# Optimization experiments

Hardware: AMD Instinct MI355X
Metric: run time of the kernel (lower is better)

The kernel has to match this reference:

```python
import jax, jax.numpy as jnp
import numpy as np

NU, NI, D, B, L, E = 100000, 50000, 128, 3, 2, 1500000
N = NU + NI  # total nodes
EPS = 1e-5


def setup_inputs() -> dict:
    key = jax.random.key(0)
    ks = jax.random.split(key, 20)
    s = 0.05  # xavier-ish scale for 128-dim layers
    inp = {}
    inp["edge_index"] = jax.random.randint(ks[0], (2, E), 0, N, dtype=jnp.int32)
    inp["edge_type"] = jax.random.randint(ks[1], (E,), 0, B, dtype=jnp.int32)
    inp["item_feats"] = jax.random.normal(ks[2], (NI, D), jnp.float32)
    inp["user_emb"] = jax.random.normal(ks[3], (NU, D), jnp.float32) * s
    inp["user_proj_W"] = jax.random.normal(ks[4], (D, D), jnp.float32) * s
    inp["user_proj_b"] = jnp.zeros((D,), jnp.float32)
    inp["item_proj_W"] = jax.random.normal(ks[5], (D, D), jnp.float32) * s
    inp["item_proj_b"] = jnp.zeros((D,), jnp.float32)
    # stacked SAGEConv params: lin_l (neighbor, with bias) and lin_r (root, no bias)
    inp["sage_Wl"] = jax.random.normal(ks[6], (B, L, D, D), jnp.float32) * s
    inp["sage_bl"] = jnp.zeros((B, L, D), jnp.float32)
    inp["sage_Wr"] = jax.random.normal(ks[7], (B, L, D, D), jnp.float32) * s
    inp["bn_gamma"] = jnp.ones((B, L, D), jnp.float32)
    inp["bn_beta"] = jnp.zeros((B, L, D), jnp.float32)
    inp["query_W"] = jax.random.normal(ks[8], (D, D), jnp.float32) * s
    inp["query_b"] = jnp.zeros((D,), jnp.float32)
    inp["key_W"] = jax.random.normal(ks[9], (B, D, D), jnp.float32) * s
    inp["key_b"] = jnp.zeros((B, D), jnp.float32)
    inp["fuse_W"] = jax.random.normal(ks[10], (D, D), jnp.float32) * s
    inp["fuse_b"] = jnp.zeros((D,), jnp.float32)
    inp["refine_W"] = jax.random.normal(ks[11], (D, D), jnp.float32) * s
    inp["refine_b"] = jnp.zeros((D,), jnp.float32)
    return inp


def reference(edge_index, edge_type, item_feats, user_emb,
              user_proj_W, user_proj_b, item_proj_W, item_proj_b,
              sage_Wl, sage_bl, sage_Wr, bn_gamma, bn_beta,
              query_W, query_b, key_W, key_b,
              fuse_W, fuse_b, refine_W, refine_b):
    # initial node features: projected user embeddings + projected item feats
    x = jnp.concatenate([user_emb @ user_proj_W + user_proj_b,
                         item_feats @ item_proj_W + item_proj_b], axis=0)  # [N, D]
    src, dst = edge_index[0], edge_index[1]
    outs = []
    for b in range(B):
        # redirect edges of other behaviours to a dummy segment N (dropped)
        dst_b = jnp.where(edge_type == b, dst, N)
        cnt = jax.ops.segment_sum(jnp.ones((E,), x.dtype), dst_b, num_segments=N + 1)[:N]
        denom = jnp.maximum(cnt, 1.0)[:, None]
        h = x
        for l in range(L):
            # SAGEConv: mean-aggregate neighbor messages + root transform
            agg = jax.ops.segment_sum(h[src], dst_b, num_segments=N + 1)[:N] / denom
            h = agg @ sage_Wl[b, l] + sage_bl[b, l] + h @ sage_Wr[b, l]
            # BatchNorm1d (training-mode batch statistics, biased variance)
            mu = h.mean(axis=0)
            var = h.var(axis=0)
            h = (h - mu) * jax.lax.rsqrt(var + EPS) * bn_gamma[b, l] + bn_beta[b, l]
            if l < L - 1:
                h = jax.nn.relu(h)
        outs.append(x + h)  # residual
    stack = jnp.stack(outs, axis=0)  # [B, N, D]
    # attention fusion across behaviours
    Q = x @ query_W + query_b                                   # [N, D]
    K = jnp.einsum('bnd,bde->bne', stack, key_W) + key_b[:, None, :]  # [B, N, D]
    logits = jnp.einsum('nd,bnd->nb', Q, K)                      # [N, B]
    w = jax.nn.softmax(logits, axis=-1)
    fused = jnp.einsum('nb,bnd->nd', w, stack)
    fused = fused @ fuse_W + fuse_b
    # refine: Linear + ReLU (dropout is identity in eval)
    return jax.nn.relu(fused @ refine_W + refine_b)
```

## Files before the change

kernel.cpp:

```cpp
#include <hip/hip_runtime.h>

#define NUSER 100000
#define NITEM 50000
#define NNODE 150000
#define DIM 128
#define NB 3
#define NL 2
#define BN_EPS 1e-5f
#define NT3P 450560
#define SCAN_BLOCKS 440
#define TILESN 2344
#define BNBLK 18750
#define BNABLK 9375

typedef unsigned short u16;
typedef _Float16 f16;
typedef __attribute__((ext_vector_type(8))) _Float16 f16x8;
typedef __attribute__((ext_vector_type(8))) unsigned short us8;
typedef __attribute__((ext_vector_type(4))) float f32x4;

__device__ __forceinline__ float h2f(u16 u) { f16 h; __builtin_memcpy(&h, &u, 2); return (float)h; }
__device__ __forceinline__ u16 f2h(float f) { f16 h = (f16)f; u16 u; __builtin_memcpy(&u, &h, 2); return u; }

struct Out3 { u16* p[3]; };
struct WPtrs { const float* s[8]; };


__global__ __launch_bounds__(256) void count_edges(const int* __restrict__ ei,
                                                   const int* __restrict__ et, int E,
                                                   int* __restrict__ cnt) {
    int t = blockIdx.x * 256 + threadIdx.x;
    if (t >= E) return;
    atomicAdd(&cnt[et[t] * NNODE + ei[E + t]], 1);
}

__global__ __launch_bounds__(256) void scan1(const int* __restrict__ cnt, int* __restrict__ bsum) {
    __shared__ int sh[256];
    int tid = threadIdx.x;
    int base = blockIdx.x * 1024 + tid * 4;
    int4 v = *(const int4*)(cnt + base);
    sh[tid] = v.x + v.y + v.z + v.w;
    __syncthreads();
    for (int off = 128; off > 0; off >>= 1) {
        if (tid < off) sh[tid] += sh[tid + off];
        __syncthreads();
    }
    if (tid == 0) bsum[blockIdx.x] = sh[0];
}

__global__ __launch_bounds__(512) void scan2(int* __restrict__ bsum, int nb) {
    __shared__ int sh[512];
    int tid = threadIdx.x;
    sh[tid] = (tid < nb) ? bsum[tid] : 0;
    __syncthreads();
    for (int off = 1; off < 512; off <<= 1) {
        int v = sh[tid];
        int add = (tid >= off) ? sh[tid - off] : 0;
        __syncthreads();
        sh[tid] = v + add;
        __syncthreads();
    }
    if (tid < nb) bsum[tid] = (tid == 0) ? 0 : sh[tid - 1];
}

__global__ __launch_bounds__(256) void scan3(const int* __restrict__ cnt, const int* __restrict__ bsum,
                                             int* __restrict__ row_start, int* __restrict__ cur) {
    __shared__ int sh[256];
    int tid = threadIdx.x;
    int base = blockIdx.x * 1024 + tid * 4;
    int4 v = *(const int4*)(cnt + base);
    sh[tid] = v.x + v.y + v.z + v.w;
    __syncthreads();
    for (int off = 1; off < 256; off <<= 1) {
        int a = sh[tid];
        int add = (tid >= off) ? sh[tid - off] : 0;
        __syncthreads();
        sh[tid] = a + add;
        __syncthreads();
    }
    int excl = ((tid == 0) ? 0 : sh[tid - 1]) + bsum[blockIdx.x];
    int4 o;
    o.x = excl; o.y = excl + v.x; o.z = o.y + v.y; o.w = o.z + v.z;
    *(int4*)(row_start + base) = o;
    *(int4*)(cur + base) = o;
}

__global__ __launch_bounds__(256) void scatter_csr(const int* __restrict__ ei,
                                                   const int* __restrict__ et, int E,
                                                   int* __restrict__ cur, int* __restrict__ adj) {
    int t = blockIdx.x * 256 + threadIdx.x;
    if (t >= E) return;
    int pos = atomicAdd(&cur[et[t] * NNODE + ei[E + t]], 1);
    adj[pos] = ei[t];
}


__global__ __launch_bounds__(256) void wconv_all(WPtrs w, u16* __restrict__ dst) {
    int gid = blockIdx.x * 256 + threadIdx.x;
    if (gid >= 20 * 16384) return;
    int m = gid >> 14, idx = gid & 16383;
    int k = idx & 127, n = idx >> 7;
    const float* src; int li;
    if (m == 0)       { src = w.s[0]; li = 0; }
    else if (m == 1)  { src = w.s[1]; li = 0; }
    else if (m < 8)   { src = w.s[2]; li = m - 2; }
    else if (m < 14)  { src = w.s[3]; li = m - 8; }
    else if (m == 14) { src = w.s[4]; li = 0; }
    else if (m < 18)  { src = w.s[5]; li = m - 15; }
    else if (m == 18) { src = w.s[6]; li = 0; }
    else              { src = w.s[7]; li = 0; }
    dst[(size_t)m * 16384 + idx] = f2h(src[(size_t)li * 16384 + k * 128 + n]);
}


__global__ __launch_bounds__(256) void bn_apply(u16* __restrict__ h,
                                                const float* __restrict__ stats6,
                                                const float* __restrict__ gamma,
                                                const float* __restrict__ beta) {
    __shared__ float sc[DIM];
    __shared__ float sf[DIM];
    const int tid = threadIdx.x;
    const int b = blockIdx.x / BNABLK;
    const int blk = blockIdx.x % BNABLK;
    const int bl = b * NL;
    if (tid < DIM) {
        const float* st = stats6 + bl * 256;
        const float invN = 1.0f / (float)NNODE;
        float mu = st[tid] * invN;
        float var = fmaxf(st[DIM + tid] * invN - mu * mu, 0.f);
        float scv = gamma[bl * DIM + tid] * rsqrtf(var + BN_EPS);
        sc[tid] = scv;
        sf[tid] = beta[bl * DIM + tid] - mu * scv;
    }
    __syncthreads();
    const int i = blk * 256 + tid;
    const int c8 = (i & 15) * 8;
    u16* p = h + (size_t)b * NNODE * DIM + (size_t)i * 8;
    us8 u = *(const us8*)p;
    us8 o;
#pragma unroll
    for (int j = 0; j < 8; ++j)
        o[j] = f2h(fmaxf(h2f(u[j]) * sc[c8 + j] + sf[c8 + j], 0.f));
    *(us8*)p = o;
}


__global__ __launch_bounds__(256, 5) void sage_layer(
    const u16* __restrict__ hin0, const u16* __restrict__ wt_Wl,
    const u16* __restrict__ wt_Wr, const float* __restrict__ sage_bl,
    float* __restrict__ stats6, Out3 outs, int layer,
    const int* __restrict__ adj, const int* __restrict__ row_start,
    const int* __restrict__ cnt) {
    __shared__ u16 T1[64][136];
    __shared__ float sstat[256];
    const int tid = threadIdx.x;
    const int b = blockIdx.x / TILESN;
    const int tile = blockIdx.x % TILESN;
    const int r0 = tile * 64;
    const int bl = b * NL + layer;
    const u16* hin = hin0 + (layer ? (size_t)b * NNODE * DIM : 0);
    const u16* Wl = wt_Wl + (size_t)bl * 16384;
    const u16* Wr = wt_Wr + (size_t)bl * 16384;

    sstat[tid] = 0.f;

    {
        const int row = tid >> 2;
        const int c0 = (tid & 3) * 32;
        float a[32];
#pragma unroll
        for (int j = 0; j < 32; ++j) a[j] = 0.f;
        const int n = r0 + row;
        if (n < NNODE) {
            const int base = b * NNODE + n;
            const int s0 = row_start[base];
            const int deg = cnt[base];
            int e = 0;
            for (; e + 1 < deg; e += 2) {
                const u16* p1 = hin + (size_t)adj[s0 + e] * DIM + c0;
                const u16* p2 = hin + (size_t)adj[s0 + e + 1] * DIM + c0;
                us8 u0 = *(const us8*)p1;
                us8 u1 = *(const us8*)(p1 + 8);
                us8 u2 = *(const us8*)(p1 + 16);
                us8 u3 = *(const us8*)(p1 + 24);
                us8 v0 = *(const us8*)p2;
                us8 v1 = *(const us8*)(p2 + 8);
                us8 v2 = *(const us8*)(p2 + 16);
                us8 v3 = *(const us8*)(p2 + 24);
#pragma unroll
                for (int j = 0; j < 8; ++j) {
                    a[j]      += h2f(u0[j]) + h2f(v0[j]);
                    a[8 + j]  += h2f(u1[j]) + h2f(v1[j]);
                    a[16 + j] += h2f(u2[j]) + h2f(v2[j]);
                    a[24 + j] += h2f(u3[j]) + h2f(v3[j]);
                }
            }
            if (e < deg) {
                const u16* p1 = hin + (size_t)adj[s0 + e] * DIM + c0;
                us8 u0 = *(const us8*)p1;
                us8 u1 = *(const us8*)(p1 + 8);
                us8 u2 = *(const us8*)(p1 + 16);
                us8 u3 = *(const us8*)(p1 + 24);
#pragma unroll
                for (int j = 0; j < 8; ++j) {
                    a[j]      += h2f(u0[j]);
                    a[8 + j]  += h2f(u1[j]);
                    a[16 + j] += h2f(u2[j]);
                    a[24 + j] += h2f(u3[j]);
                }
            }
            const float s = 1.0f / (float)(deg > 1 ? deg : 1);
#pragma unroll
            for (int j = 0; j < 32; ++j) a[j] *= s;
        }
#pragma unroll
        for (int k = 0; k < 4; ++k) {
            us8 o;
#pragma unroll
            for (int j = 0; j < 8; ++j) o[j] = f2h(a[8 * k + j]);
            *(us8*)&T1[row][c0 + 8 * k] = o;
        }
    }
    __syncthreads();

    const int wave = tid >> 6, lane = tid & 63, q = lane >> 4, rlo = lane & 15;
    const f16x8 zf = (f16x8)(f16)0.f;
    f32x4 acc[4][2];
#pragma unroll
    for (int t = 0; t < 4; ++t) { acc[t][0] = (f32x4)0.f; acc[t][1] = (f32x4)0.f; }
#pragma unroll
    for (int kc = 0; kc < DIM; kc += 32) {
        f16x8 b1v[2], b2v[2];
#pragma unroll
        for (int c = 0; c < 2; ++c) {
            b1v[c] = *(const f16x8*)(Wl + (size_t)(wave * 32 + 16 * c + rlo) * DIM + kc + q * 8);
            b2v[c] = *(const f16x8*)(Wr + (size_t)(wave * 32 + 16 * c + rlo) * DIM + kc + q * 8);
        }
#pragma unroll
        for (int t = 0; t < 4; ++t) {
            f16x8 a1 = *(const f16x8*)&T1[16 * t + rlo][kc + q * 8];
            int rr = r0 + 16 * t + rlo;
            f16x8 a2 = (rr < NNODE) ? *(const f16x8*)(hin + (size_t)rr * DIM + kc + q * 8) : zf;
            acc[t][0] = __builtin_amdgcn_mfma_f32_16x16x32_f16(a1, b1v[0], acc[t][0], 0, 0, 0);
            acc[t][1] = __builtin_amdgcn_mfma_f32_16x16x32_f16(a1, b1v[1], acc[t][1], 0, 0, 0);
            acc[t][0] = __builtin_amdgcn_mfma_f32_16x16x32_f16(a2, b2v[0], acc[t][0], 0, 0, 0);
            acc[t][1] = __builtin_amdgcn_mfma_f32_16x16x32_f16(a2, b2v[1], acc[t][1], 0, 0, 0);
        }
    }

    const int col0 = wave * 32 + rlo, col1 = col0 + 16;
    const float bb0 = sage_bl[bl * DIM + col0], bb1 = sage_bl[bl * DIM + col1];
    u16* C = outs.p[b];
    float rs0 = 0, rq0 = 0, rs1 = 0, rq1 = 0;
#pragma unroll
    for (int t = 0; t < 4; ++t) {
#pragma unroll
        for (int r = 0; r < 4; ++r) {
            int row = r0 + 16 * t + q * 4 + r;
            if (row >= NNODE) continue;
            float v0 = acc[t][0][r] + bb0;
            float v1 = acc[t][1][r] + bb1;
            rs0 += v0; rq0 += v0 * v0; rs1 += v1; rq1 += v1 * v1;
            C[(size_t)row * DIM + col0] = f2h(v0);
            C[(size_t)row * DIM + col1] = f2h(v1);
        }
    }
    rs0 += __shfl_xor(rs0, 16); rs0 += __shfl_xor(rs0, 32);
    rq0 += __shfl_xor(rq0, 16); rq0 += __shfl_xor(rq0, 32);
    rs1 += __shfl_xor(rs1, 16); rs1 += __shfl_xor(rs1, 32);
    rq1 += __shfl_xor(rq1, 16); rq1 += __shfl_xor(rq1, 32);
    if (q == 0) {
        atomicAdd(&sstat[col0], rs0);
        atomicAdd(&sstat[DIM + col0], rq0);
        atomicAdd(&sstat[col1], rs1);
        atomicAdd(&sstat[DIM + col1], rq1);
    }
    __syncthreads();
    if (tid < DIM) {
        float* so = stats6 + bl * 256;
        atomicAdd(&so[tid], sstat[tid]);
        atomicAdd(&so[DIM + tid], sstat[DIM + tid]);
    }
}


__global__ __launch_bounds__(256) void bn_final(Out3 ins, const float* __restrict__ stats6,
                                                const float* __restrict__ gamma,
                                                const float* __restrict__ beta,
                                                const u16* __restrict__ xh,
                                                u16* __restrict__ stackb) {
    int blk = blockIdx.x;
    int b = blk / BNBLK;
    int t = (blk % BNBLK) * 256 + threadIdx.x;
    int n = t >> 5;
    int d = (t & 31) * 4;
    const int bl = b * NL + 1;
    const float invN = 1.0f / (float)NNODE;
    const float* st = stats6 + bl * 256;
    float4 s = *(const float4*)&st[d];
    float4 sq = *(const float4*)&st[DIM + d];
    float4 g = *(const float4*)&gamma[bl * DIM + d];
    float4 be = *(const float4*)&beta[bl * DIM + d];
    float mx = s.x * invN, my = s.y * invN, mz = s.z * invN, mw = s.w * invN;
    float cx = g.x * rsqrtf(fmaxf(sq.x * invN - mx * mx, 0.f) + BN_EPS);
    float cy = g.y * rsqrtf(fmaxf(sq.y * invN - my * my, 0.f) + BN_EPS);
    float cz = g.z * rsqrtf(fmaxf(sq.z * invN - mz * mz, 0.f) + BN_EPS);
    float cw = g.w * rsqrtf(fmaxf(sq.w * invN - mw * mw, 0.f) + BN_EPS);
    size_t off = (size_t)n * DIM + d;
    ushort4 hv = *(const ushort4*)(ins.p[b] + off);
    ushort4 xv = *(const ushort4*)(xh + off);
    ushort4 o;
    o.x = f2h((h2f(hv.x) - mx) * cx + be.x + h2f(xv.x));
    o.y = f2h((h2f(hv.y) - my) * cy + be.y + h2f(xv.y));
    o.z = f2h((h2f(hv.z) - mz) * cz + be.z + h2f(xv.z));
    o.w = f2h((h2f(hv.w) - mw) * cw + be.w + h2f(xv.w));
    *(ushort4*)(stackb + (size_t)b * NNODE * DIM + off) = o;
}


__global__ __launch_bounds__(256) void gemm_p(
    const void* __restrict__ Av, const u16* __restrict__ Wt,
    const float* __restrict__ bias, void* __restrict__ Cv, int M, int tiles,
    const float* __restrict__ Qf, float* __restrict__ logits, int flags) {
    int bi = 0, tile = blockIdx.x;
    if (flags & 128) { bi = blockIdx.x / tiles; tile = blockIdx.x % tiles; }
    const u16* A16 = (const u16*)Av + ((flags & 128) ? (size_t)bi * NNODE * DIM : 0);
    const float* A32 = (const float*)Av;
    const u16* W = Wt + (size_t)bi * 16384;
    const float* bs = bias + bi * DIM;
    const int r0 = tile * 64;
    const int tid = threadIdx.x;
    const int wave = tid >> 6, lane = tid & 63, q = lane >> 4, rlo = lane & 15;
    f32x4 acc[4][2];
#pragma unroll
    for (int t = 0; t < 4; ++t) { acc[t][0] = (f32x4)0.f; acc[t][1] = (f32x4)0.f; }
    const f16x8 zf = (f16x8)(f16)0.f;
#pragma unroll
    for (int kc = 0; kc < DIM; kc += 32) {
        f16x8 av[4], bv[2];
#pragma unroll
        for (int t = 0; t < 4; ++t) {
            int row = r0 + 16 * t + rlo;
            if (row < M) {
                if (flags & 8) {
                    const float* p = A32 + (size_t)row * DIM + kc + q * 8;
                    float4 x0 = *(const float4*)p;
                    float4 x1 = *(const float4*)(p + 4);
                    f16x8 tmp;
                    tmp[0] = (f16)x0.x; tmp[1] = (f16)x0.y; tmp[2] = (f16)x0.z; tmp[3] = (f16)x0.w;
                    tmp[4] = (f16)x1.x; tmp[5] = (f16)x1.y; tmp[6] = (f16)x1.z; tmp[7] = (f16)x1.w;
                    av[t] = tmp;
                } else {
                    av[t] = *(const f16x8*)(A16 + (size_t)row * DIM + kc + q * 8);
                }
            } else {
                av[t] = zf;
            }
        }
#pragma unroll
        for (int c = 0; c < 2; ++c)
            bv[c] = *(const f16x8*)(W + (size_t)(wave * 32 + 16 * c + rlo) * DIM + kc + q * 8);
#pragma unroll
        for (int t = 0; t < 4; ++t) {
            acc[t][0] = __builtin_amdgcn_mfma_f32_16x16x32_f16(av[t], bv[0], acc[t][0], 0, 0, 0);
            acc[t][1] = __builtin_amdgcn_mfma_f32_16x16x32_f16(av[t], bv[1], acc[t][1], 0, 0, 0);
        }
    }

    const int col0 = wave * 32 + rlo, col1 = col0 + 16;
    const float bb0 = bs[col0], bb1 = bs[col1];

    if (flags & 64) {
#pragma unroll
        for (int t = 0; t < 4; ++t) {
#pragma unroll
            for (int r = 0; r < 4; ++r) {
                int row = r0 + 16 * t + q * 4 + r;
                if (row < M) {
                    float v = (acc[t][0][r] + bb0) * Qf[(size_t)row * DIM + col0]
                            + (acc[t][1][r] + bb1) * Qf[(size_t)row * DIM + col1];
                    v += __shfl_xor(v, 1);
                    v += __shfl_xor(v, 2);
                    v += __shfl_xor(v, 4);
                    v += __shfl_xor(v, 8);
                    if (rlo == 0) atomicAdd(&logits[row * NB + bi], v);
                }
            }
        }
        return;
    }

#pragma unroll
    for (int t = 0; t < 4; ++t) {
#pragma unroll
        for (int r = 0; r < 4; ++r) {
            int row = r0 + 16 * t + q * 4 + r;
            if (row >= M) continue;
            float v0 = acc[t][0][r] + bb0;
            float v1 = acc[t][1][r] + bb1;
            if (flags & 1) { v0 = fmaxf(v0, 0.f); v1 = fmaxf(v1, 0.f); }
            if (flags & 32) {
                ((u16*)Cv)[(size_t)row * DIM + col0] = f2h(v0);
                ((u16*)Cv)[(size_t)row * DIM + col1] = f2h(v1);
            } else {
                ((float*)Cv)[(size_t)row * DIM + col0] = v0;
                ((float*)Cv)[(size_t)row * DIM + col1] = v1;
            }
        }
    }
}


__global__ __launch_bounds__(256) void fuse_gemm(
    const u16* __restrict__ stk, const float* __restrict__ logits,
    const u16* __restrict__ Wt, const float* __restrict__ bias,
    u16* __restrict__ C) {
    __shared__ u16 T[64][136];
    const int tid = threadIdx.x;
    const int r0 = blockIdx.x * 64;
    for (int i = tid; i < 1024; i += 256) {
        int r = i >> 4, c8 = (i & 15) * 8;
        int n = r0 + r;
        us8 o;
        if (n < NNODE) {
            float l0 = logits[n * NB + 0];
            float l1 = logits[n * NB + 1];
            float l2 = logits[n * NB + 2];
            float mm = fmaxf(l0, fmaxf(l1, l2));
            float e0 = expf(l0 - mm), e1 = expf(l1 - mm), e2 = expf(l2 - mm);
            float inv = 1.0f / (e0 + e1 + e2);
            float w0 = e0 * inv, w1 = e1 * inv, w2 = e2 * inv;
            size_t off = (size_t)n * DIM + c8;
            us8 u0 = *(const us8*)(stk + off);
            us8 u1 = *(const us8*)(stk + (size_t)NNODE * DIM + off);
            us8 u2 = *(const us8*)(stk + (size_t)2 * NNODE * DIM + off);
#pragma unroll
            for (int j = 0; j < 8; ++j)
                o[j] = f2h(w0 * h2f(u0[j]) + w1 * h2f(u1[j]) + w2 * h2f(u2[j]));
        } else {
            o = (us8)(u16)0;
        }
        *(us8*)&T[r][c8] = o;
    }
    __syncthreads();

    const int wave = tid >> 6, lane = tid & 63, q = lane >> 4, rlo = lane & 15;
    f32x4 acc[4][2];
#pragma unroll
    for (int t = 0; t < 4; ++t) { acc[t][0] = (f32x4)0.f; acc[t][1] = (f32x4)0.f; }
#pragma unroll
    for (int kc = 0; kc < DIM; kc += 32) {
        f16x8 av[4], bv[2];
#pragma unroll
        for (int t = 0; t < 4; ++t)
            av[t] = *(const f16x8*)&T[16 * t + rlo][kc + q * 8];
#pragma unroll
        for (int c = 0; c < 2; ++c)
            bv[c] = *(const f16x8*)(Wt + (size_t)(wave * 32 + 16 * c + rlo) * DIM + kc + q * 8);
#pragma unroll
        for (int t = 0; t < 4; ++t) {
            acc[t][0] = __builtin_amdgcn_mfma_f32_16x16x32_f16(av[t], bv[0], acc[t][0], 0, 0, 0);
            acc[t][1] = __builtin_amdgcn_mfma_f32_16x16x32_f16(av[t], bv[1], acc[t][1], 0, 0, 0);
        }
    }
    const int col0 = wave * 32 + rlo, col1 = col0 + 16;
    const float bb0 = bias[col0], bb1 = bias[col1];
#pragma unroll
    for (int t = 0; t < 4; ++t) {
#pragma unroll
        for (int r = 0; r < 4; ++r) {
            int row = r0 + 16 * t + q * 4 + r;
            if (row >= NNODE) continue;
            C[(size_t)row * DIM + col0] = f2h(acc[t][0][r] + bb0);
            C[(size_t)row * DIM + col1] = f2h(acc[t][1][r] + bb1);
        }
    }
}


extern "C" void kernel_launch(void* const* d_in, const int* in_sizes, int n_in,
                              void* d_out, int out_size, void* d_ws, size_t ws_size,
                              hipStream_t stream) {
    const int* edge_index    = (const int*)d_in[0];
    const int* edge_type     = (const int*)d_in[1];
    const float* item_feats  = (const float*)d_in[2];
    const float* user_emb    = (const float*)d_in[3];
    const float* user_proj_b = (const float*)d_in[5];
    const float* item_proj_b = (const float*)d_in[7];
    const float* sage_bl  = (const float*)d_in[9];
    const float* bn_gamma = (const float*)d_in[11];
    const float* bn_beta  = (const float*)d_in[12];
    const float* query_b  = (const float*)d_in[14];
    const float* key_b    = (const float*)d_in[16];
    const float* fuse_b   = (const float*)d_in[18];
    const float* refine_b = (const float*)d_in[20];
    const int E = in_sizes[1];

    const size_t ND = (size_t)NNODE * DIM;
    char* w = (char*)d_ws;
    u16* xh = (u16*)w;          w += ND * 2;
    u16* stackb = (u16*)w;      w += NB * ND * 2;
    u16* fbuf = (u16*)w;        w += ND * 2;
    int* cnt = (int*)w;         w += (size_t)NT3P * 4;
    int* row_start = (int*)w;   w += (size_t)NT3P * 4;
    int* cur = (int*)w;         w += (size_t)NT3P * 4;
    int* adj = (int*)w;         w += (size_t)E * 4;
    float* logits = (float*)w;  w += (size_t)NNODE * NB * 4;
    u16* wt = (u16*)w;          w += (size_t)20 * 16384 * 2;
    int* bsum = (int*)w;        w += 2048;
    float* stats6 = (float*)w;  w += 6 * 256 * 4;

    const u16* wt_user = wt;
    const u16* wt_item = wt + 16384;
    const u16* wt_Wl   = wt + 2 * 16384;
    const u16* wt_Wr   = wt + 8 * 16384;
    const u16* wt_q    = wt + 14 * 16384;
    const u16* wt_key  = wt + 15 * 16384;
    const u16* wt_fuse = wt + 18 * 16384;
    const u16* wt_ref  = wt + 19 * 16384;

    u16* dout16 = (u16*)d_out;
    float* Qf = (float*)d_out;

    hipMemsetAsync(cnt, 0, (size_t)NT3P * 4, stream);
    hipMemsetAsync(logits, 0, (size_t)NNODE * NB * 4, stream);
    hipMemsetAsync(stats6, 0, 6 * 256 * 4, stream);
    int gE = (E + 255) / 256;
    count_edges<<<gE, 256, 0, stream>>>(edge_index, edge_type, E, cnt);
    scan1<<<SCAN_BLOCKS, 256, 0, stream>>>(cnt, bsum);
    scan2<<<1, 512, 0, stream>>>(bsum, SCAN_BLOCKS);
    scan3<<<SCAN_BLOCKS, 256, 0, stream>>>(cnt, bsum, row_start, cur);
    scatter_csr<<<gE, 256, 0, stream>>>(edge_index, edge_type, E, cur, adj);

    WPtrs wp;
    wp.s[0] = (const float*)d_in[4];
    wp.s[1] = (const float*)d_in[6];
    wp.s[2] = (const float*)d_in[8];
    wp.s[3] = (const float*)d_in[10];
    wp.s[4] = (const float*)d_in[13];
    wp.s[5] = (const float*)d_in[15];
    wp.s[6] = (const float*)d_in[17];
    wp.s[7] = (const float*)d_in[19];
    wconv_all<<<1280, 256, 0, stream>>>(wp, wt);

    const int TU = (NUSER + 63) / 64, TI = (NITEM + 63) / 64;
    gemm_p<<<TU, 256, 0, stream>>>(user_emb, wt_user, user_proj_b, xh,
                                   NUSER, TU, nullptr, nullptr, 8 | 32);
    gemm_p<<<TI, 256, 0, stream>>>(item_feats, wt_item, item_proj_b, xh + (size_t)NUSER * DIM,
                                   NITEM, TI, nullptr, nullptr, 8 | 32);

    Out3 out_l0, out_l1;
    for (int b = 0; b < NB; ++b) out_l0.p[b] = stackb + (size_t)b * ND;
    out_l1.p[0] = fbuf;
    out_l1.p[1] = dout16;
    out_l1.p[2] = dout16 + ND;

    sage_layer<<<NB * TILESN, 256, 0, stream>>>(xh, wt_Wl, wt_Wr, sage_bl,
                                                stats6, out_l0, 0,
                                                adj, row_start, cnt);
    bn_apply<<<NB * BNABLK, 256, 0, stream>>>(stackb, stats6, bn_gamma, bn_beta);
    sage_layer<<<NB * TILESN, 256, 0, stream>>>(stackb, wt_Wl, wt_Wr, sage_bl,
                                                stats6, out_l1, 1,
                                                adj, row_start, cnt);
    bn_final<<<NB * BNBLK, 256, 0, stream>>>(out_l1, stats6, bn_gamma, bn_beta,
                                             xh, stackb);

    gemm_p<<<TILESN, 256, 0, stream>>>(xh, wt_q, query_b, Qf,
                                       NNODE, TILESN, nullptr, nullptr, 0);
    gemm_p<<<NB * TILESN, 256, 0, stream>>>(stackb, wt_key, key_b, nullptr,
                                            NNODE, TILESN, Qf, logits, 64 | 128);
    fuse_gemm<<<TILESN, 256, 0, stream>>>(stackb, logits, wt_fuse, fuse_b, fbuf);
    gemm_p<<<TILESN, 256, 0, stream>>>(fbuf, wt_ref, refine_b, d_out,
                                       NNODE, TILESN, nullptr, nullptr, 1);
}
```

Measured before the change: 1.142 ms.

## Fuse final BN, attention, fuse and refine GEMMs into one tiled kernel

Replaces bn_final, the query GEMM, the key/logit GEMM, fuse_gemm and the refine GEMM with a single attn_fuse kernel. Per 64-row tile it applies the final BatchNorm plus residual into shared memory and computes Q, the per-behaviour logits, the softmax and the fused and refined outputs, all on-chip. This removes the stack, Q, logits and intermediate fused-buffer round trips through global memory. Layer-1 SAGE outputs for behaviours 1 and 2 are written tile-interleaved into the output buffer, with a separate tail buffer for the last tile, so they are not overwritten before being read. The gather loop is also unrolled to 4 edges and occupancy is lowered to 4 blocks per CU, which trades registers for more loads in flight. The fused kernel carries large shared memory (3 tiles) and long serial per-block work, which may reduce occupancy.

```diff
diff --git a/kernel.cpp b/kernel.cpp
--- a/kernel.cpp
+++ b/kernel.cpp
@@ -10,7 +10,6 @@
 #define NT3P 450560
 #define SCAN_BLOCKS 440
 #define TILESN 2344
-#define BNBLK 18750
 #define BNABLK 9375
 
 typedef unsigned short u16;
@@ -145,7 +144,7 @@
 }
 
 
-__global__ __launch_bounds__(256, 5) void sage_layer(
+__global__ __launch_bounds__(256, 4) void sage_layer(
     const u16* __restrict__ hin0, const u16* __restrict__ wt_Wl,
     const u16* __restrict__ wt_Wr, const float* __restrict__ sage_bl,
     float* __restrict__ stats6, Out3 outs, int layer,
@@ -176,17 +175,36 @@
             const int s0 = row_start[base];
             const int deg = cnt[base];
             int e = 0;
-            for (; e + 1 < deg; e += 2) {
+            for (; e + 3 < deg; e += 4) {
+                const int i0 = adj[s0 + e],     i1 = adj[s0 + e + 1];
+                const int i2 = adj[s0 + e + 2], i3 = adj[s0 + e + 3];
+                const u16* p0 = hin + (size_t)i0 * DIM + c0;
+                const u16* p1 = hin + (size_t)i1 * DIM + c0;
+                const u16* p2 = hin + (size_t)i2 * DIM + c0;
+                const u16* p3 = hin + (size_t)i3 * DIM + c0;
+                us8 u00 = *(const us8*)p0,        u01 = *(const us8*)(p0 + 8);
+                us8 u02 = *(const us8*)(p0 + 16), u03 = *(const us8*)(p0 + 24);
+                us8 u10 = *(const us8*)p1,        u11 = *(const us8*)(p1 + 8);
+                us8 u12 = *(const us8*)(p1 + 16), u13 = *(const us8*)(p1 + 24);
+                us8 u20 = *(const us8*)p2,        u21 = *(const us8*)(p2 + 8);
+                us8 u22 = *(const us8*)(p2 + 16), u23 = *(const us8*)(p2 + 24);
+                us8 u30 = *(const us8*)p3,        u31 = *(const us8*)(p3 + 8);
+                us8 u32 = *(const us8*)(p3 + 16), u33 = *(const us8*)(p3 + 24);
+#pragma unroll
+                for (int j = 0; j < 8; ++j) {
+                    a[j]      += (h2f(u00[j]) + h2f(u10[j])) + (h2f(u20[j]) + h2f(u30[j]));
+                    a[8 + j]  += (h2f(u01[j]) + h2f(u11[j])) + (h2f(u21[j]) + h2f(u31[j]));
+                    a[16 + j] += (h2f(u02[j]) + h2f(u12[j])) + (h2f(u22[j]) + h2f(u32[j]));
+                    a[24 + j] += (h2f(u03[j]) + h2f(u13[j])) + (h2f(u23[j]) + h2f(u33[j]));
+                }
+            }
+            if (e + 1 < deg) {
                 const u16* p1 = hin + (size_t)adj[s0 + e] * DIM + c0;
                 const u16* p2 = hin + (size_t)adj[s0 + e + 1] * DIM + c0;
-                us8 u0 = *(const us8*)p1;
-                us8 u1 = *(const us8*)(p1 + 8);
-                us8 u2 = *(const us8*)(p1 + 16);
-                us8 u3 = *(const us8*)(p1 + 24);
-                us8 v0 = *(const us8*)p2;
-                us8 v1 = *(const us8*)(p2 + 8);
-                us8 v2 = *(const us8*)(p2 + 16);
-                us8 v3 = *(const us8*)(p2 + 24);
+                us8 u0 = *(const us8*)p1,        u1 = *(const us8*)(p1 + 8);
+                us8 u2 = *(const us8*)(p1 + 16), u3 = *(const us8*)(p1 + 24);
+                us8 v0 = *(const us8*)p2,        v1 = *(const us8*)(p2 + 8);
+                us8 v2 = *(const us8*)(p2 + 16), v3 = *(const us8*)(p2 + 24);
 #pragma unroll
                 for (int j = 0; j < 8; ++j) {
                     a[j]      += h2f(u0[j]) + h2f(v0[j]);
@@ -194,13 +212,12 @@
                     a[16 + j] += h2f(u2[j]) + h2f(v2[j]);
                     a[24 + j] += h2f(u3[j]) + h2f(v3[j]);
                 }
+                e += 2;
             }
             if (e < deg) {
                 const u16* p1 = hin + (size_t)adj[s0 + e] * DIM + c0;
-                us8 u0 = *(const us8*)p1;
-                us8 u1 = *(const us8*)(p1 + 8);
-                us8 u2 = *(const us8*)(p1 + 16);
-                us8 u3 = *(const us8*)(p1 + 24);
+                us8 u0 = *(const us8*)p1,        u1 = *(const us8*)(p1 + 8);
+                us8 u2 = *(const us8*)(p1 + 16), u3 = *(const us8*)(p1 + 24);
 #pragma unroll
                 for (int j = 0; j < 8; ++j) {
                     a[j]      += h2f(u0[j]);
@@ -250,19 +267,29 @@
 
     const int col0 = wave * 32 + rlo, col1 = col0 + 16;
     const float bb0 = sage_bl[bl * DIM + col0], bb1 = sage_bl[bl * DIM + col1];
-    u16* C = outs.p[b];
+    const bool tiled = (layer == 1) && (b > 0);
+    u16* Cb;
+    if (!tiled) {
+        Cb = outs.p[b];
+    } else {
+        Cb = ((tile == TILESN - 1) ? outs.p[2]
+                                   : outs.p[1] + (size_t)tile * 16384)
+             + (size_t)(b - 1) * 8192;
+    }
     float rs0 = 0, rq0 = 0, rs1 = 0, rq1 = 0;
 #pragma unroll
     for (int t = 0; t < 4; ++t) {
 #pragma unroll
         for (int r = 0; r < 4; ++r) {
-            int row = r0 + 16 * t + q * 4 + r;
+            int rloc = 16 * t + q * 4 + r;
+            int row = r0 + rloc;
             if (row >= NNODE) continue;
             float v0 = acc[t][0][r] + bb0;
             float v1 = acc[t][1][r] + bb1;
             rs0 += v0; rq0 += v0 * v0; rs1 += v1; rq1 += v1 * v1;
-            C[(size_t)row * DIM + col0] = f2h(v0);
-            C[(size_t)row * DIM + col1] = f2h(v1);
+            size_t off = tiled ? (size_t)rloc * DIM : (size_t)row * DIM;
+            Cb[off + col0] = f2h(v0);
+            Cb[off + col1] = f2h(v1);
         }
     }
     rs0 += __shfl_xor(rs0, 16); rs0 += __shfl_xor(rs0, 32);
@@ -284,51 +311,222 @@
 }
 
 
-__global__ __launch_bounds__(256) void bn_final(Out3 ins, const float* __restrict__ stats6,
-                                                const float* __restrict__ gamma,
-                                                const float* __restrict__ beta,
-                                                const u16* __restrict__ xh,
-                                                u16* __restrict__ stackb) {
-    int blk = blockIdx.x;
-    int b = blk / BNBLK;
-    int t = (blk % BNBLK) * 256 + threadIdx.x;
-    int n = t >> 5;
-    int d = (t & 31) * 4;
-    const int bl = b * NL + 1;
-    const float invN = 1.0f / (float)NNODE;
-    const float* st = stats6 + bl * 256;
-    float4 s = *(const float4*)&st[d];
-    float4 sq = *(const float4*)&st[DIM + d];
-    float4 g = *(const float4*)&gamma[bl * DIM + d];
-    float4 be = *(const float4*)&beta[bl * DIM + d];
-    float mx = s.x * invN, my = s.y * invN, mz = s.z * invN, mw = s.w * invN;
-    float cx = g.x * rsqrtf(fmaxf(sq.x * invN - mx * mx, 0.f) + BN_EPS);
-    float cy = g.y * rsqrtf(fmaxf(sq.y * invN - my * my, 0.f) + BN_EPS);
-    float cz = g.z * rsqrtf(fmaxf(sq.z * invN - mz * mz, 0.f) + BN_EPS);
-    float cw = g.w * rsqrtf(fmaxf(sq.w * invN - mw * mw, 0.f) + BN_EPS);
-    size_t off = (size_t)n * DIM + d;
-    ushort4 hv = *(const ushort4*)(ins.p[b] + off);
-    ushort4 xv = *(const ushort4*)(xh + off);
-    ushort4 o;
-    o.x = f2h((h2f(hv.x) - mx) * cx + be.x + h2f(xv.x));
-    o.y = f2h((h2f(hv.y) - my) * cy + be.y + h2f(xv.y));
-    o.z = f2h((h2f(hv.z) - mz) * cz + be.z + h2f(xv.z));
-    o.w = f2h((h2f(hv.w) - mw) * cw + be.w + h2f(xv.w));
-    *(ushort4*)(stackb + (size_t)b * NNODE * DIM + off) = o;
+__global__ __launch_bounds__(256) void attn_fuse(
+    const u16* __restrict__ hpre0, const u16* __restrict__ hpre12,
+    const u16* __restrict__ tailb, const float* __restrict__ stats6,
+    const float* __restrict__ gamma, const float* __restrict__ beta,
+    const u16* __restrict__ xh, const u16* __restrict__ wt,
+    const float* __restrict__ query_b, const float* __restrict__ key_b,
+    const float* __restrict__ fuse_b, const float* __restrict__ refine_b,
+    float* __restrict__ out) {
+    __shared__ __attribute__((aligned(16))) u16 St[3][64][136];
+    __shared__ float sc[3][DIM], sf[3][DIM];
+    __shared__ float slog[64][4];
+    __shared__ float swt[64][4];
+    const int tid = threadIdx.x;
+    const int tile = blockIdx.x;
+    const int r0 = tile * 64;
+    const u16* wt_q    = wt + 14 * 16384;
+    const u16* wt_key  = wt + 15 * 16384;
+    const u16* wt_fuse = wt + 18 * 16384;
+    const u16* wt_ref  = wt + 19 * 16384;
+
+    if (tid < DIM) {
+        const float invN = 1.0f / (float)NNODE;
+#pragma unroll
+        for (int b = 0; b < NB; ++b) {
+            const int bl = b * NL + 1;
+            const float* st = stats6 + bl * 256;
+            float mu = st[tid] * invN;
+            float var = fmaxf(st[DIM + tid] * invN - mu * mu, 0.f);
+            float c = gamma[bl * DIM + tid] * rsqrtf(var + BN_EPS);
+            sc[b][tid] = c;
+            sf[b][tid] = beta[bl * DIM + tid] - mu * c;
+        }
+    }
+    if (tid < 64) { slog[tid][0] = 0.f; slog[tid][1] = 0.f; slog[tid][2] = 0.f; }
+    __syncthreads();
+
+    for (int i = tid; i < 1024; i += 256) {
+        int r = i >> 4, c8 = (i & 15) * 8;
+        int n = r0 + r;
+        if (n < NNODE) {
+            us8 xv = *(const us8*)(xh + (size_t)n * DIM + c8);
+#pragma unroll
+            for (int b = 0; b < NB; ++b) {
+                const u16* src = (b == 0)
+                    ? hpre0 + (size_t)n * DIM + c8
+                    : ((tile == TILESN - 1) ? tailb : hpre12 + (size_t)tile * 16384)
+                      + (size_t)(b - 1) * 8192 + r * DIM + c8;
+                us8 hv = *(const us8*)src;
+                us8 o;
+#pragma unroll
+                for (int j = 0; j < 8; ++j)
+                    o[j] = f2h(h2f(hv[j]) * sc[b][c8 + j] + sf[b][c8 + j] + h2f(xv[j]));
+                *(us8*)&St[b][r][c8] = o;
+            }
+        } else {
+            us8 z = (us8)(u16)0;
+#pragma unroll
+            for (int b = 0; b < NB; ++b) *(us8*)&St[b][r][c8] = z;
+        }
+    }
+    __syncthreads();
+
+    const int wave = tid >> 6, lane = tid & 63, q = lane >> 4, rlo = lane & 15;
+    const int col0 = wave * 32 + rlo, col1 = col0 + 16;
+    const f16x8 zf = (f16x8)(f16)0.f;
+
+    f32x4 qa[4][2];
+#pragma unroll
+    for (int t = 0; t < 4; ++t) { qa[t][0] = (f32x4)0.f; qa[t][1] = (f32x4)0.f; }
+#pragma unroll
+    for (int kc = 0; kc < DIM; kc += 32) {
+        f16x8 bv0 = *(const f16x8*)(wt_q + (size_t)(wave * 32 + rlo) * DIM + kc + q * 8);
+        f16x8 bv1 = *(const f16x8*)(wt_q + (size_t)(wave * 32 + 16 + rlo) * DIM + kc + q * 8);
+#pragma unroll
+        for (int t = 0; t < 4; ++t) {
+            int rr = r0 + 16 * t + rlo;
+            f16x8 av = (rr < NNODE) ? *(const f16x8*)(xh + (size_t)rr * DIM + kc + q * 8) : zf;
+            qa[t][0] = __builtin_amdgcn_mfma_f32_16x16x32_f16(av, bv0, qa[t][0], 0, 0, 0);
+            qa[t][1] = __builtin_amdgcn_mfma_f32_16x16x32_f16(av, bv1, qa[t][1], 0, 0, 0);
+        }
+    }
+    {
+        const float qb0 = query_b[col0], qb1 = query_b[col1];
+#pragma unroll
+        for (int t = 0; t < 4; ++t)
+#pragma unroll
+            for (int r = 0; r < 4; ++r) { qa[t][0][r] += qb0; qa[t][1][r] += qb1; }
+    }
+
+#pragma unroll
+    for (int b = 0; b < NB; ++b) {
+        f32x4 ka[4][2];
+#pragma unroll
+        for (int t = 0; t < 4; ++t) { ka[t][0] = (f32x4)0.f; ka[t][1] = (f32x4)0.f; }
+        const u16* Wk = wt_key + (size_t)b * 16384;
+#pragma unroll
+        for (int kc = 0; kc < DIM; kc += 32) {
+            f16x8 bv0 = *(const f16x8*)(Wk + (size_t)(wave * 32 + rlo) * DIM + kc + q * 8);
+            f16x8 bv1 = *(const f16x8*)(Wk + (size_t)(wave * 32 + 16 + rlo) * DIM + kc + q * 8);
+#pragma unroll
+            for (int t = 0; t < 4; ++t) {
+                f16x8 av = *(const f16x8*)&St[b][16 * t + rlo][kc + q * 8];
+                ka[t][0] = __builtin_amdgcn_mfma_f32_16x16x32_f16(av, bv0, ka[t][0], 0, 0, 0);
+                ka[t][1] = __builtin_amdgcn_mfma_f32_16x16x32_f16(av, bv1, ka[t][1], 0, 0, 0);
+            }
+        }
+        const float kb0 = key_b[b * DIM + col0], kb1 = key_b[b * DIM + col1];
+#pragma unroll
+        for (int t = 0; t < 4; ++t) {
+#pragma unroll
+            for (int r = 0; r < 4; ++r) {
+                int rloc = 16 * t + q * 4 + r;
+                float v = (ka[t][0][r] + kb0) * qa[t][0][r]
+                        + (ka[t][1][r] + kb1) * qa[t][1][r];
+                v += __shfl_xor(v, 1);
+                v += __shfl_xor(v, 2);
+                v += __shfl_xor(v, 4);
+                v += __shfl_xor(v, 8);
+                if (rlo == 0) atomicAdd(&slog[rloc][b], v);
+            }
+        }
+    }
+    __syncthreads();
+
+    if (tid < 64) {
+        float l0 = slog[tid][0], l1 = slog[tid][1], l2 = slog[tid][2];
+        float mm = fmaxf(l0, fmaxf(l1, l2));
+        float e0 = expf(l0 - mm), e1 = expf(l1 - mm), e2 = expf(l2 - mm);
+        float inv = 1.0f / (e0 + e1 + e2);
+        swt[tid][0] = e0 * inv; swt[tid][1] = e1 * inv; swt[tid][2] = e2 * inv;
+    }
+    __syncthreads();
+
+    f32x4 facc[4][2];
+#pragma unroll
+    for (int t = 0; t < 4; ++t) { facc[t][0] = (f32x4)0.f; facc[t][1] = (f32x4)0.f; }
+#pragma unroll
+    for (int b = 0; b < NB; ++b) {
+        f32x4 ga[4][2];
+#pragma unroll
+        for (int t = 0; t < 4; ++t) { ga[t][0] = (f32x4)0.f; ga[t][1] = (f32x4)0.f; }
+#pragma unroll
+        for (int kc = 0; kc < DIM; kc += 32) {
+            f16x8 bv0 = *(const f16x8*)(wt_fuse + (size_t)(wave * 32 + rlo) * DIM + kc + q * 8);
+            f16x8 bv1 = *(const f16x8*)(wt_fuse + (size_t)(wave * 32 + 16 + rlo) * DIM + kc + q * 8);
+#pragma unroll
+            for (int t = 0; t < 4; ++t) {
+                f16x8 av = *(const f16x8*)&St[b][16 * t + rlo][kc + q * 8];
+                ga[t][0] = __builtin_amdgcn_mfma_f32_16x16x32_f16(av, bv0, ga[t][0], 0, 0, 0);
+                ga[t][1] = __builtin_amdgcn_mfma_f32_16x16x32_f16(av, bv1, ga[t][1], 0, 0, 0);
+            }
+        }
+#pragma unroll
+        for (int t = 0; t < 4; ++t) {
+#pragma unroll
+            for (int r = 0; r < 4; ++r) {
+                int rloc = 16 * t + q * 4 + r;
+                float wgt = swt[rloc][b];
+                facc[t][0][r] += wgt * ga[t][0][r];
+                facc[t][1][r] += wgt * ga[t][1][r];
+            }
+        }
+    }
+    __syncthreads();
+
+    {
+        const float fb0 = fuse_b[col0], fb1 = fuse_b[col1];
+#pragma unroll
+        for (int t = 0; t < 4; ++t) {
+#pragma unroll
+            for (int r = 0; r < 4; ++r) {
+                int rloc = 16 * t + q * 4 + r;
+                St[0][rloc][col0] = f2h(facc[t][0][r] + fb0);
+                St[0][rloc][col1] = f2h(facc[t][1][r] + fb1);
+            }
+        }
+    }
+    __syncthreads();
+
+    f32x4 racc[4][2];
+#pragma unroll
+    for (int t = 0; t < 4; ++t) { racc[t][0] = (f32x4)0.f; racc[t][1] = (f32x4)0.f; }
+#pragma unroll
+    for (int kc = 0; kc < DIM; kc += 32) {
+        f16x8 bv0 = *(const f16x8*)(wt_ref + (size_t)(wave * 32 + rlo) * DIM + kc + q * 8);
+        f16x8 bv1 = *(const f16x8*)(wt_ref + (size_t)(wave * 32 + 16 + rlo) * DIM + kc + q * 8);
+#pragma unroll
+        for (int t = 0; t < 4; ++t) {
+            f16x8 av = *(const f16x8*)&St[0][16 * t + rlo][kc + q * 8];
+            racc[t][0] = __builtin_amdgcn_mfma_f32_16x16x32_f16(av, bv0, racc[t][0], 0, 0, 0);
+            racc[t][1] = __builtin_amdgcn_mfma_f32_16x16x32_f16(av, bv1, racc[t][1], 0, 0, 0);
+        }
+    }
+    {
+        const float rb0 = refine_b[col0], rb1 = refine_b[col1];
+#pragma unroll
+        for (int t = 0; t < 4; ++t) {
+#pragma unroll
+            for (int r = 0; r < 4; ++r) {
+                int row = r0 + 16 * t + q * 4 + r;
+                if (row >= NNODE) continue;
+                out[(size_t)row * DIM + col0] = fmaxf(racc[t][0][r] + rb0, 0.f);
+                out[(size_t)row * DIM + col1] = fmaxf(racc[t][1][r] + rb1, 0.f);
+            }
+        }
+    }
 }
 
 
 __global__ __launch_bounds__(256) void gemm_p(
     const void* __restrict__ Av, const u16* __restrict__ Wt,
-    const float* __restrict__ bias, void* __restrict__ Cv, int M, int tiles,
-    const float* __restrict__ Qf, float* __restrict__ logits, int flags) {
-    int bi = 0, tile = blockIdx.x;
-    if (flags & 128) { bi = blockIdx.x / tiles; tile = blockIdx.x % tiles; }
-    const u16* A16 = (const u16*)Av + ((flags & 128) ? (size_t)bi * NNODE * DIM : 0);
+    const float* __restrict__ bias, void* __restrict__ Cv, int M, int flags) {
+    const u16* A16 = (const u16*)Av;
     const float* A32 = (const float*)Av;
-    const u16* W = Wt + (size_t)bi * 16384;
-    const float* bs = bias + bi * DIM;
-    const int r0 = tile * 64;
+    const float* bs = bias;
+    const int r0 = blockIdx.x * 64;
     const int tid = threadIdx.x;
     const int wave = tid >> 6, lane = tid & 63, q = lane >> 4, rlo = lane & 15;
     f32x4 acc[4][2];
@@ -359,7 +557,7 @@
         }
 #pragma unroll
         for (int c = 0; c < 2; ++c)
-            bv[c] = *(const f16x8*)(W + (size_t)(wave * 32 + 16 * c + rlo) * DIM + kc + q * 8);
+            bv[c] = *(const f16x8*)(Wt + (size_t)(wave * 32 + 16 * c + rlo) * DIM + kc + q * 8);
 #pragma unroll
         for (int t = 0; t < 4; ++t) {
             acc[t][0] = __builtin_amdgcn_mfma_f32_16x16x32_f16(av[t], bv[0], acc[t][0], 0, 0, 0);
@@ -369,27 +567,6 @@
 
     const int col0 = wave * 32 + rlo, col1 = col0 + 16;
     const float bb0 = bs[col0], bb1 = bs[col1];
-
-    if (flags & 64) {
-#pragma unroll
-        for (int t = 0; t < 4; ++t) {
-#pragma unroll
-            for (int r = 0; r < 4; ++r) {
-                int row = r0 + 16 * t + q * 4 + r;
-                if (row < M) {
-                    float v = (acc[t][0][r] + bb0) * Qf[(size_t)row * DIM + col0]
-                            + (acc[t][1][r] + bb1) * Qf[(size_t)row * DIM + col1];
-                    v += __shfl_xor(v, 1);
-                    v += __shfl_xor(v, 2);
-                    v += __shfl_xor(v, 4);
-                    v += __shfl_xor(v, 8);
-                    if (rlo == 0) atomicAdd(&logits[row * NB + bi], v);
-                }
-            }
-        }
-        return;
-    }
-
 #pragma unroll
     for (int t = 0; t < 4; ++t) {
 #pragma unroll
@@ -406,73 +583,6 @@
                 ((float*)Cv)[(size_t)row * DIM + col0] = v0;
                 ((float*)Cv)[(size_t)row * DIM + col1] = v1;
             }
-        }
-    }
-}
-
-
-__global__ __launch_bounds__(256) void fuse_gemm(
-    const u16* __restrict__ stk, const float* __restrict__ logits,
-    const u16* __restrict__ Wt, const float* __restrict__ bias,
-    u16* __restrict__ C) {
-    __shared__ u16 T[64][136];
-    const int tid = threadIdx.x;
-    const int r0 = blockIdx.x * 64;
-    for (int i = tid; i < 1024; i += 256) {
-        int r = i >> 4, c8 = (i & 15) * 8;
-        int n = r0 + r;
-        us8 o;
-        if (n < NNODE) {
-            float l0 = logits[n * NB + 0];
-            float l1 = logits[n * NB + 1];
-            float l2 = logits[n * NB + 2];
-            float mm = fmaxf(l0, fmaxf(l1, l2));
-            float e0 = expf(l0 - mm), e1 = expf(l1 - mm), e2 = expf(l2 - mm);
-            float inv = 1.0f / (e0 + e1 + e2);
-            float w0 = e0 * inv, w1 = e1 * inv, w2 = e2 * inv;
-            size_t off = (size_t)n * DIM + c8;
-            us8 u0 = *(const us8*)(stk + off);
-            us8 u1 = *(const us8*)(stk + (size_t)NNODE * DIM + off);
-            us8 u2 = *(const us8*)(stk + (size_t)2 * NNODE * DIM + off);
-#pragma unroll
-            for (int j = 0; j < 8; ++j)
-                o[j] = f2h(w0 * h2f(u0[j]) + w1 * h2f(u1[j]) + w2 * h2f(u2[j]));
-        } else {
-            o = (us8)(u16)0;
-        }
-        *(us8*)&T[r][c8] = o;
-    }
-    __syncthreads();
-
-    const int wave = tid >> 6, lane = tid & 63, q = lane >> 4, rlo = lane & 15;
-    f32x4 acc[4][2];
-#pragma unroll
-    for (int t = 0; t < 4; ++t) { acc[t][0] = (f32x4)0.f; acc[t][1] = (f32x4)0.f; }
-#pragma unroll
-    for (int kc = 0; kc < DIM; kc += 32) {
-        f16x8 av[4], bv[2];
-#pragma unroll
-        for (int t = 0; t < 4; ++t)
-            av[t] = *(const f16x8*)&T[16 * t + rlo][kc + q * 8];
-#pragma unroll
-        for (int c = 0; c < 2; ++c)
-            bv[c] = *(const f16x8*)(Wt + (size_t)(wave * 32 + 16 * c + rlo) * DIM + kc + q * 8);
-#pragma unroll
-        for (int t = 0; t < 4; ++t) {
-            acc[t][0] = __builtin_amdgcn_mfma_f32_16x16x32_f16(av[t], bv[0], acc[t][0], 0, 0, 0);
-            acc[t][1] = __builtin_amdgcn_mfma_f32_16x16x32_f16(av[t], bv[1], acc[t][1], 0, 0, 0);
-        }
-    }
-    const int col0 = wave * 32 + rlo, col1 = col0 + 16;
-    const float bb0 = bias[col0], bb1 = bias[col1];
-#pragma unroll
-    for (int t = 0; t < 4; ++t) {
-#pragma unroll
-        for (int r = 0; r < 4; ++r) {
-            int row = r0 + 16 * t + q * 4 + r;
-            if (row >= NNODE) continue;
-            C[(size_t)row * DIM + col0] = f2h(acc[t][0][r] + bb0);
-            C[(size_t)row * DIM + col1] = f2h(acc[t][1][r] + bb1);
         }
     }
 }
@@ -505,25 +615,19 @@
     int* row_start = (int*)w;   w += (size_t)NT3P * 4;
     int* cur = (int*)w;         w += (size_t)NT3P * 4;
     int* adj = (int*)w;         w += (size_t)E * 4;
-    float* logits = (float*)w;  w += (size_t)NNODE * NB * 4;
     u16* wt = (u16*)w;          w += (size_t)20 * 16384 * 2;
     int* bsum = (int*)w;        w += 2048;
     float* stats6 = (float*)w;  w += 6 * 256 * 4;
+    u16* tailb = (u16*)w;       w += 32768;
 
     const u16* wt_user = wt;
     const u16* wt_item = wt + 16384;
     const u16* wt_Wl   = wt + 2 * 16384;
     const u16* wt_Wr   = wt + 8 * 16384;
-    const u16* wt_q    = wt + 14 * 16384;
-    const u16* wt_key  = wt + 15 * 16384;
-    const u16* wt_fuse = wt + 18 * 16384;
-    const u16* wt_ref  = wt + 19 * 16384;
 
     u16* dout16 = (u16*)d_out;
-    float* Qf = (float*)d_out;
 
     hipMemsetAsync(cnt, 0, (size_t)NT3P * 4, stream);
-    hipMemsetAsync(logits, 0, (size_t)NNODE * NB * 4, stream);
     hipMemsetAsync(stats6, 0, 6 * 256 * 4, stream);
     int gE = (E + 255) / 256;
     count_edges<<<gE, 256, 0, stream>>>(edge_index, edge_type, E, cnt);
@@ -544,16 +648,15 @@
     wconv_all<<<1280, 256, 0, stream>>>(wp, wt);
 
     const int TU = (NUSER + 63) / 64, TI = (NITEM + 63) / 64;
-    gemm_p<<<TU, 256, 0, stream>>>(user_emb, wt_user, user_proj_b, xh,
-                                   NUSER, TU, nullptr, nullptr, 8 | 32);
-    gemm_p<<<TI, 256, 0, stream>>>(item_feats, wt_item, item_proj_b, xh + (size_t)NUSER * DIM,
-                                   NITEM, TI, nullptr, nullptr, 8 | 32);
+    gemm_p<<<TU, 256, 0, stream>>>(user_emb, wt_user, user_proj_b, xh, NUSER, 8 | 32);
+    gemm_p<<<TI, 256, 0, stream>>>(item_feats, wt_item, item_proj_b,
+                                   xh + (size_t)NUSER * DIM, NITEM, 8 | 32);
 
     Out3 out_l0, out_l1;
     for (int b = 0; b < NB; ++b) out_l0.p[b] = stackb + (size_t)b * ND;
     out_l1.p[0] = fbuf;
     out_l1.p[1] = dout16;
-    out_l1.p[2] = dout16 + ND;
+    out_l1.p[2] = tailb;
 
     sage_layer<<<NB * TILESN, 256, 0, stream>>>(xh, wt_Wl, wt_Wr, sage_bl,
                                                 stats6, out_l0, 0,
@@ -562,14 +665,9 @@
     sage_layer<<<NB * TILESN, 256, 0, stream>>>(stackb, wt_Wl, wt_Wr, sage_bl,
                                                 stats6, out_l1, 1,
                                                 adj, row_start, cnt);
-    bn_final<<<NB * BNBLK, 256, 0, stream>>>(out_l1, stats6, bn_gamma, bn_beta,
-                                             xh, stackb);
-
-    gemm_p<<<TILESN, 256, 0, stream>>>(xh, wt_q, query_b, Qf,
-                                       NNODE, TILESN, nullptr, nullptr, 0);
-    gemm_p<<<NB * TILESN, 256, 0, stream>>>(stackb, wt_key, key_b, nullptr,
-                                            NNODE, TILESN, Qf, logits, 64 | 128);
-    fuse_gemm<<<TILESN, 256, 0, stream>>>(stackb, logits, wt_fuse, fuse_b, fbuf);
-    gemm_p<<<TILESN, 256, 0, stream>>>(fbuf, wt_ref, refine_b, d_out,
-                                       NNODE, TILESN, nullptr, nullptr, 1);
-}
+
+    attn_fuse<<<TILESN, 256, 0, stream>>>(fbuf, dout16, tailb, stats6,
+                                          bn_gamma, bn_beta, xh, wt,
+                                          query_b, key_b, fuse_b, refine_b,
+                                          (float*)d_out);
+}
```

After: 1.009 ms. 1.13x faster.
